# Performance work log

Hardware: AMD Instinct MI355X
Metric: run time of the kernel (lower is better)

Reference implementation:

```python
import jax, jax.numpy as jnp
import numpy as np

HEADS = 8
DIM_HEAD = 64
WINDOW = 512
SCALE = DIM_HEAD ** -0.5


def setup_inputs() -> dict:
    key = jax.random.key(0)
    k1, k2, k3 = jax.random.split(key, 3)
    b, dim, n = 2, 256, 32768
    hidden = HEADS * DIM_HEAD  # 512
    x = jax.random.normal(k1, (b, dim, n), dtype=jnp.float32)
    # Conv1d(dim, hidden*3, 1, bias=False) weight -> [3*hidden, dim]
    w_qkv = jax.random.normal(k2, (3 * hidden, dim), dtype=jnp.float32) * (dim ** -0.5)
    # Conv1d(hidden, dim, 1) weight/bias
    w_out = jax.random.normal(k3, (dim, hidden), dtype=jnp.float32) * (hidden ** -0.5)
    b_out = jnp.zeros((dim,), dtype=jnp.float32)
    return {"x": x, "w_qkv": w_qkv, "w_out": w_out, "b_out": b_out}


def reference(x, w_qkv, w_out, b_out):
    b, c, n = x.shape
    h, d, w = HEADS, DIM_HEAD, WINDOW
    nw = n // w  # n chosen divisible by window size
    # 1x1 conv == channel matmul
    qkv = jnp.einsum('oc,bcn->bon', w_qkv, x)  # [b, 3*h*d, n]
    q, k, v = jnp.split(qkv, 3, axis=1)
    # [b, h, d, nw, w]
    def to_windows(t):
        return t.reshape(b, h, d, nw, w)
    q = to_windows(q) * SCALE
    k = to_windows(k)
    v = to_windows(v)
    # non-overlapping local windows: block-diagonal attention
    sim = jnp.einsum('bhdni,bhdnj->bhnij', q, k)        # [b,h,nw,w,w]
    attn = jax.nn.softmax(sim, axis=-1)
    out = jnp.einsum('bhnij,bhdnj->bhdni', attn, v)      # [b,h,d,nw,w]
    out = out.reshape(b, h * d, n)
    return jnp.einsum('oc,bcn->bon', w_out, out) + b_out[None, :, None]
```

## Files before the change

kernel.cpp:

```cpp
#include <hip/hip_runtime.h>
#include <stdint.h>
#include <stddef.h>


typedef _Float16 f16;
typedef _Float16 half8 __attribute__((ext_vector_type(8)));
typedef float f32x4 __attribute__((ext_vector_type(4)));

#define NSEQ 32768
#define NTOT 65536
#define WIN  512

__device__ __forceinline__ void async_copy16(const f16* g, f16* l) {
  __builtin_amdgcn_global_load_lds(
      (const __attribute__((address_space(1))) void*)g,
      (__attribute__((address_space(3))) void*)l, 16, 0, 0);
}

__device__ __forceinline__ int packrtz(float a, float b) {
  typedef __fp16 fp16v2 __attribute__((ext_vector_type(2)));
  fp16v2 h = __builtin_amdgcn_cvt_pkrtz(a, b);
  return __builtin_bit_cast(int, h);
}

__global__ __launch_bounds__(256) void convert_w(
    const float* __restrict__ wqkv, const float* __restrict__ wout,
    f16* __restrict__ wqh, f16* __restrict__ woh) {
  int idx = blockIdx.x * 256 + threadIdx.x;
  if (idx < 1536 * 256) {
    float v = wqkv[idx];
    if (idx < 512 * 256) v *= 0.18033688011112042f;
    wqh[idx] = (f16)v;
  } else {
    int j = idx - 1536 * 256;
    if (j < 256 * 512) woh[j] = (f16)wout[j];
  }
}

__global__ __launch_bounds__(256) void transpose_x(
    const float* __restrict__ x, f16* __restrict__ xT) {
  __shared__ alignas(16) float tile[32][33];
  const int tx = threadIdx.x & 31, ty = threadIdx.x >> 5;
  const int bx = blockIdx.x, by = blockIdx.y;
  const float* xb = x + (size_t)blockIdx.z * 256 * NSEQ;
  f16* xTb = xT + (size_t)blockIdx.z * NSEQ * 256;
#pragma unroll
  for (int r = 0; r < 4; ++r) {
    int c = by * 32 + ty + r * 8;
    int n = bx * 32 + tx;
    tile[ty + r * 8][tx] = xb[(size_t)c * NSEQ + n];
  }
  __syncthreads();
  const int tx16 = threadIdx.x & 15, ty16 = threadIdx.x >> 4;
#pragma unroll
  for (int r = 0; r < 2; ++r) {
    int n = bx * 32 + ty16 + r * 16;
    int c = by * 32 + tx16 * 2;
    union {
      f16 h[2];
      int i;
    } u;
    u.h[0] = (f16)tile[tx16 * 2][ty16 + r * 16];
    u.h[1] = (f16)tile[tx16 * 2 + 1][ty16 + r * 16];
    *(int*)(xTb + (size_t)n * 256 + c) = u.i;
  }
}

template <int MODE, int SWZ>
__global__ __launch_bounds__(256) void gemm_k(
    const f16* __restrict__ A, const f16* __restrict__ Bm,
    void* __restrict__ outp, const float* __restrict__ bias, int K,
    int bstride, int ostride) {
  __shared__ alignas(16) f16 As[2][8192];
  __shared__ alignas(16) f16 Bs[2][8192];
  const int tid = threadIdx.x;
  const int lane = tid & 63, wid = tid >> 6;
  const int quad = lane >> 4, lid = lane & 15;

  int colb, rowb;
  if (SWZ) {
    int lin = blockIdx.y * 8 + blockIdx.x;
    int x = lin & 7, s = lin >> 3;
    colb = s & 7;
    rowb = x * 64 + (s >> 3);
  } else {
    colb = blockIdx.x;
    rowb = blockIdx.y;
  }
  const int row0 = rowb * 128, col0 = colb * 128;
  const int wm = (wid >> 1) * 64, wn = (wid & 1) * 64;

  f32x4 acc[4][4];
  const f32x4 zero = {0.f, 0.f, 0.f, 0.f};
#pragma unroll
  for (int i = 0; i < 4; ++i)
#pragma unroll
    for (int j = 0; j < 4; ++j) acc[i][j] = zero;

  const int kIters = K >> 6;

  auto stage = [&](int kt, int buf) {
    const int k0 = kt * 64;
#pragma unroll
    for (int rd = 0; rd < 4; ++rd) {
      int slot = rd * 256 + tid;
      int r = slot & 127, kc = slot >> 7;
      async_copy16(A + (size_t)(row0 + r) * K + k0 + kc * 8,
                   &As[buf][slot * 8]);
      async_copy16(Bm + (size_t)(col0 + r) * bstride + k0 + kc * 8,
                   &Bs[buf][slot * 8]);
    }
  };

  stage(0, 0);
  int p = 0;
  for (int kt = 0; kt < kIters; ++kt) {
    __syncthreads();
    if (kt + 1 < kIters) stage(kt + 1, p ^ 1);

    half8 af[2][4], bf[2][4];
#pragma unroll
    for (int ks = 0; ks < 2; ++ks) {
#pragma unroll
      for (int mi = 0; mi < 4; ++mi)
        af[ks][mi] = *(const half8*)(&As[p][((ks * 4 + quad) * 128 + wm +
                                             mi * 16 + lid) * 8]);
#pragma unroll
      for (int ni = 0; ni < 4; ++ni)
        bf[ks][ni] = *(const half8*)(&Bs[p][((ks * 4 + quad) * 128 + wn +
                                             ni * 16 + lid) * 8]);
    }
#pragma unroll
    for (int ks = 0; ks < 2; ++ks)
#pragma unroll
      for (int mi = 0; mi < 4; ++mi)
#pragma unroll
        for (int ni = 0; ni < 4; ++ni)
          acc[mi][ni] = __builtin_amdgcn_mfma_f32_16x16x32_f16(
              af[ks][mi], bf[ks][ni], acc[mi][ni], 0, 0, 0);
    p ^= 1;
  }

#pragma unroll
  for (int mi = 0; mi < 4; ++mi) {
#pragma unroll
    for (int r = 0; r < 4; ++r) {
      int grow = row0 + wm + mi * 16 + quad * 4 + r;
#pragma unroll
      for (int ni = 0; ni < 4; ++ni) {
        int gcol = col0 + wn + ni * 16 + lid;
        float v = acc[mi][ni][r];
        if (MODE == 2) {
          ((float*)outp)[(size_t)(gcol >> 15) * (256u * 32768u) +
                         (size_t)grow * 32768 + (gcol & 32767)] =
              v + bias[grow];
        } else {
          ((f16*)outp)[(size_t)grow * ostride + gcol] = (f16)v;
        }
      }
    }
  }
}

__global__ __launch_bounds__(512, 2) void attn_k(
    const f16* __restrict__ qk, const f16* __restrict__ vws,
    f16* __restrict__ ows) {
  __shared__ alignas(16) f16 smem[16384];

  const int tid = threadIdx.x;
  const int lane = tid & 63, wid = tid >> 6;
  const int quad = lane >> 4, lid = lane & 15;
  const int win = blockIdx.x;
  const int h = blockIdx.y;
  const size_t nbase = (size_t)blockIdx.z * NSEQ + (size_t)win * WIN;
  const int iw0 = wid * 64;

  half8 aq[4][2];
#pragma unroll
  for (int ig = 0; ig < 4; ++ig)
#pragma unroll
    for (int ks = 0; ks < 2; ++ks)
      aq[ig][ks] = *(const half8*)(qk + (nbase + iw0 + ig * 16 + lid) * 1024 +
                                   h * 64 + ks * 32 + quad * 8);

  f32x4 OT[4][4];
  const f32x4 zero = {0.f, 0.f, 0.f, 0.f};
#pragma unroll
  for (int di = 0; di < 4; ++di)
#pragma unroll
    for (int ig = 0; ig < 4; ++ig) OT[di][ig] = zero;
  float l_run[4] = {0.f, 0.f, 0.f, 0.f};

  const int sa = tid & 63, sc = tid >> 6;
  const int psa = (sa & 32) | ((sa & 12) << 1) | ((sa >> 2) & 4) | (sa & 3);

  async_copy16(qk + (nbase + psa) * 1024 + 512 + h * 64 + sc * 8,
               smem + tid * 8);
  async_copy16(vws + (size_t)(h * 64 + sa) * NTOT + nbase + sc * 8,
               smem + 4096 + tid * 8);

  int p = 0;
  for (int jt = 0; jt < 8; ++jt) {
    __syncthreads();
    if (jt < 7) {
      const int j0n = (jt + 1) * 64;
      f16* Kb = smem + (1 - p) * 8192;
      async_copy16(qk + (nbase + j0n + psa) * 1024 + 512 + h * 64 + sc * 8,
                   Kb + tid * 8);
      async_copy16(vws + (size_t)(h * 64 + sa) * NTOT + nbase + j0n + sc * 8,
                   Kb + 4096 + tid * 8);
    }
    const f16* Ks = smem + p * 8192;
    const f16* Vs = smem + p * 8192 + 4096;

    f32x4 sT[4][4];
#pragma unroll
    for (int jg = 0; jg < 4; ++jg)
#pragma unroll
      for (int ig = 0; ig < 4; ++ig) sT[jg][ig] = zero;
#pragma unroll
    for (int ks = 0; ks < 2; ++ks)
#pragma unroll
      for (int jg = 0; jg < 4; ++jg) {
        half8 bk =
            *(const half8*)(Ks + ((ks * 4 + quad) * 64 + jg * 16 + lid) * 8);
#pragma unroll
        for (int ig = 0; ig < 4; ++ig)
          sT[jg][ig] = __builtin_amdgcn_mfma_f32_16x16x32_f16(
              bk, aq[ig][ks], sT[jg][ig], 0, 0, 0);
      }

    int pk[4][4][2];
#pragma unroll
    for (int jg = 0; jg < 4; ++jg)
#pragma unroll
      for (int ig = 0; ig < 4; ++ig) {
        float e0 = __builtin_amdgcn_exp2f(sT[jg][ig][0]);
        float e1 = __builtin_amdgcn_exp2f(sT[jg][ig][1]);
        float e2 = __builtin_amdgcn_exp2f(sT[jg][ig][2]);
        float e3 = __builtin_amdgcn_exp2f(sT[jg][ig][3]);
        l_run[ig] += (e0 + e1) + (e2 + e3);
        pk[jg][ig][0] = packrtz(e0, e1);
        pk[jg][ig][1] = packrtz(e2, e3);
      }

#pragma unroll
    for (int ks2 = 0; ks2 < 2; ++ks2) {
      const int ta = ks2 * 2, tb = ta + 1;
      half8 pt[4];
#pragma unroll
      for (int ig = 0; ig < 4; ++ig) {
        union {
          int i[4];
          half8 h;
        } u;
        u.i[0] = pk[ta][ig][0];
        u.i[1] = pk[ta][ig][1];
        u.i[2] = pk[tb][ig][0];
        u.i[3] = pk[tb][ig][1];
        pt[ig] = u.h;
      }
#pragma unroll
      for (int di = 0; di < 4; ++di) {
        half8 av =
            *(const half8*)(Vs + ((ks2 * 4 + quad) * 64 + di * 16 + lid) * 8);
#pragma unroll
        for (int ig = 0; ig < 4; ++ig)
          OT[di][ig] = __builtin_amdgcn_mfma_f32_16x16x32_f16(
              av, pt[ig], OT[di][ig], 0, 0, 0);
      }
    }
    p ^= 1;
  }

#pragma unroll
  for (int ig = 0; ig < 4; ++ig) {
    l_run[ig] += __shfl_xor(l_run[ig], 16, 64);
    l_run[ig] += __shfl_xor(l_run[ig], 32, 64);
  }

#pragma unroll
  for (int ig = 0; ig < 4; ++ig) {
    float inv = 1.0f / l_run[ig];
    size_t rowb = (nbase + iw0 + ig * 16 + lid) * 1024 + h * 64;
#pragma unroll
    for (int di = 0; di < 4; ++di) {
      int2 o;
      o.x = packrtz(OT[di][ig][0] * inv, OT[di][ig][1] * inv);
      o.y = packrtz(OT[di][ig][2] * inv, OT[di][ig][3] * inv);
      *(int2*)(ows + rowb + di * 16 + quad * 4) = o;
    }
  }
}

extern "C" void kernel_launch(void* const* d_in, const int* in_sizes, int n_in,
                              void* d_out, int out_size, void* d_ws,
                              size_t ws_size, hipStream_t stream) {
  const float* x = (const float*)d_in[0];
  const float* w_qkv = (const float*)d_in[1];
  const float* w_out = (const float*)d_in[2];
  const float* b_out = (const float*)d_in[3];

  char* ws = (char*)d_ws;
  f16* qkw = (f16*)(ws);
  f16* vw = (f16*)(ws + 134217728);
  f16* xT = (f16*)(ws + 201326592);
  f16* wqh = (f16*)(ws + 234881024);
  f16* woh = (f16*)(ws + 235667456);

  convert_w<<<2048, 256, 0, stream>>>(w_qkv, w_out, wqh, woh);
  transpose_x<<<dim3(1024, 8, 2), 256, 0, stream>>>(x, xT);
  gemm_k<0, 1><<<dim3(8, 512), 256, 0, stream>>>(xT, wqh, qkw, nullptr, 256,
                                                 256, 1024);
  gemm_k<0, 0><<<dim3(512, 4), 256, 0, stream>>>(wqh + 1024 * 256, xT, vw,
                                                 nullptr, 256, 256, NTOT);
  attn_k<<<dim3(64, 8, 2), 512, 0, stream>>>(qkw, vw, qkw);
  gemm_k<2, 0><<<dim3(512, 2), 256, 0, stream>>>(woh, qkw, d_out, b_out, 512,
                                                 1024, 0);
}
```

Measured before the change: 393.1 us.

## Split attention window across two 256-thread blocks instead of one 512-thread block

The attention kernel now launches twice as many blocks of 256 threads, and each block handles half of the query rows in a window. Each block stages the full K/V tiles itself, with two async copies per thread. This aims for finer-grained scheduling and more resident blocks per CU. The cost is that K/V for each window is loaded twice from global memory and LDS is duplicated per block.

```diff
diff --git a/kernel.cpp b/kernel.cpp
--- a/kernel.cpp
+++ b/kernel.cpp
@@ -162,7 +162,7 @@
   }
 }
 
-__global__ __launch_bounds__(512, 2) void attn_k(
+__global__ __launch_bounds__(256, 4) void attn_k(
     const f16* __restrict__ qk, const f16* __restrict__ vws,
     f16* __restrict__ ows) {
   __shared__ alignas(16) f16 smem[16384];
@@ -170,10 +170,12 @@
   const int tid = threadIdx.x;
   const int lane = tid & 63, wid = tid >> 6;
   const int quad = lane >> 4, lid = lane & 15;
-  const int win = blockIdx.x;
+  const int bx = blockIdx.x;
+  const int win = bx & 63;
+  const int half = bx >> 6;
   const int h = blockIdx.y;
   const size_t nbase = (size_t)blockIdx.z * NSEQ + (size_t)win * WIN;
-  const int iw0 = wid * 64;
+  const int iw0 = half * 256 + wid * 64;
 
   half8 aq[4][2];
 #pragma unroll
@@ -191,25 +193,26 @@
     for (int ig = 0; ig < 4; ++ig) OT[di][ig] = zero;
   float l_run[4] = {0.f, 0.f, 0.f, 0.f};
 
-  const int sa = tid & 63, sc = tid >> 6;
-  const int psa = (sa & 32) | ((sa & 12) << 1) | ((sa >> 2) & 4) | (sa & 3);
-
-  async_copy16(qk + (nbase + psa) * 1024 + 512 + h * 64 + sc * 8,
-               smem + tid * 8);
-  async_copy16(vws + (size_t)(h * 64 + sa) * NTOT + nbase + sc * 8,
-               smem + 4096 + tid * 8);
+  auto stage = [&](int j0, f16* Kb) {
+#pragma unroll
+    for (int c = 0; c < 2; ++c) {
+      int slot = c * 256 + tid;
+      int sa = slot & 63, sc = slot >> 6;
+      int psa = (sa & 32) | ((sa & 12) << 1) | ((sa >> 2) & 4) | (sa & 3);
+      async_copy16(qk + (nbase + j0 + psa) * 1024 + 512 + h * 64 + sc * 8,
+                   Kb + slot * 8);
+      async_copy16(vws + (size_t)(h * 64 + sa) * NTOT + nbase + j0 + sc * 8,
+                   Kb + 4096 + slot * 8);
+    }
+  };
+
+  stage(0, smem);
 
   int p = 0;
   for (int jt = 0; jt < 8; ++jt) {
     __syncthreads();
-    if (jt < 7) {
-      const int j0n = (jt + 1) * 64;
-      f16* Kb = smem + (1 - p) * 8192;
-      async_copy16(qk + (nbase + j0n + psa) * 1024 + 512 + h * 64 + sc * 8,
-                   Kb + tid * 8);
-      async_copy16(vws + (size_t)(h * 64 + sa) * NTOT + nbase + j0n + sc * 8,
-                   Kb + 4096 + tid * 8);
-    }
+    if (jt < 7)
+      stage((jt + 1) * 64, smem + (1 - p) * 8192);
     const f16* Ks = smem + p * 8192;
     const f16* Vs = smem + p * 8192 + 4096;
 
@@ -314,7 +317,7 @@
                                                  256, 1024);
   gemm_k<0, 0><<<dim3(512, 4), 256, 0, stream>>>(wqh + 1024 * 256, xT, vw,
                                                  nullptr, 256, 256, NTOT);
-  attn_k<<<dim3(64, 8, 2), 512, 0, stream>>>(qkw, vw, qkw);
+  attn_k<<<dim3(128, 8, 2), 256, 0, stream>>>(qkw, vw, qkw);
   gemm_k<2, 0><<<dim3(512, 2), 256, 0, stream>>>(woh, qkw, d_out, b_out, 512,
                                                  1024, 0);
 }
```

Result: slower. 766.2 us (+94.9%).

## Quad-buffer K/V tiles, two tiles per barrier, with MFMA priority hints

Applied to the files above, without the earlier changes.

Grows the attention kernel's LDS staging from two to four 64-key K/V buffers. Each barrier now prefetches the next two tiles and computes two, which halves the number of __syncthreads per window. It also wraps the MFMA sections in s_setprio to favour matrix issue over the exp/pack phase. LDS use per block doubles to 64 KB, which at 2 blocks per CU may limit occupancy.

```diff
diff --git a/kernel.cpp b/kernel.cpp
--- a/kernel.cpp
+++ b/kernel.cpp
@@ -165,7 +165,7 @@
 __global__ __launch_bounds__(512, 2) void attn_k(
     const f16* __restrict__ qk, const f16* __restrict__ vws,
     f16* __restrict__ ows) {
-  __shared__ alignas(16) f16 smem[16384];
+  __shared__ alignas(16) f16 smem[32768];
 
   const int tid = threadIdx.x;
   const int lane = tid & 63, wid = tid >> 6;
@@ -194,83 +194,92 @@
   const int sa = tid & 63, sc = tid >> 6;
   const int psa = (sa & 32) | ((sa & 12) << 1) | ((sa >> 2) & 4) | (sa & 3);
 
-  async_copy16(qk + (nbase + psa) * 1024 + 512 + h * 64 + sc * 8,
-               smem + tid * 8);
-  async_copy16(vws + (size_t)(h * 64 + sa) * NTOT + nbase + sc * 8,
-               smem + 4096 + tid * 8);
-
-  int p = 0;
-  for (int jt = 0; jt < 8; ++jt) {
+  auto stage = [&](int jt) {
+    f16* Kb = smem + (jt & 3) * 8192;
+    const int j0 = jt * 64;
+    async_copy16(qk + (nbase + j0 + psa) * 1024 + 512 + h * 64 + sc * 8,
+                 Kb + tid * 8);
+    async_copy16(vws + (size_t)(h * 64 + sa) * NTOT + nbase + j0 + sc * 8,
+                 Kb + 4096 + tid * 8);
+  };
+
+  stage(0);
+  stage(1);
+
+  for (int s = 0; s < 4; ++s) {
     __syncthreads();
-    if (jt < 7) {
-      const int j0n = (jt + 1) * 64;
-      f16* Kb = smem + (1 - p) * 8192;
-      async_copy16(qk + (nbase + j0n + psa) * 1024 + 512 + h * 64 + sc * 8,
-                   Kb + tid * 8);
-      async_copy16(vws + (size_t)(h * 64 + sa) * NTOT + nbase + j0n + sc * 8,
-                   Kb + 4096 + tid * 8);
-    }
-    const f16* Ks = smem + p * 8192;
-    const f16* Vs = smem + p * 8192 + 4096;
-
-    f32x4 sT[4][4];
-#pragma unroll
-    for (int jg = 0; jg < 4; ++jg)
-#pragma unroll
-      for (int ig = 0; ig < 4; ++ig) sT[jg][ig] = zero;
-#pragma unroll
-    for (int ks = 0; ks < 2; ++ks)
-#pragma unroll
-      for (int jg = 0; jg < 4; ++jg) {
-        half8 bk =
-            *(const half8*)(Ks + ((ks * 4 + quad) * 64 + jg * 16 + lid) * 8);
-#pragma unroll
-        for (int ig = 0; ig < 4; ++ig)
-          sT[jg][ig] = __builtin_amdgcn_mfma_f32_16x16x32_f16(
-              bk, aq[ig][ks], sT[jg][ig], 0, 0, 0);
+    if (s < 3) {
+      stage(2 * s + 2);
+      stage(2 * s + 3);
+    }
+#pragma unroll
+    for (int t = 0; t < 2; ++t) {
+      const int jt = 2 * s + t;
+      const f16* Ks = smem + (jt & 3) * 8192;
+      const f16* Vs = Ks + 4096;
+
+      f32x4 sT[4][4];
+#pragma unroll
+      for (int jg = 0; jg < 4; ++jg)
+#pragma unroll
+        for (int ig = 0; ig < 4; ++ig) sT[jg][ig] = zero;
+      __builtin_amdgcn_s_setprio(1);
+#pragma unroll
+      for (int ks = 0; ks < 2; ++ks)
+#pragma unroll
+        for (int jg = 0; jg < 4; ++jg) {
+          half8 bk =
+              *(const half8*)(Ks + ((ks * 4 + quad) * 64 + jg * 16 + lid) * 8);
+#pragma unroll
+          for (int ig = 0; ig < 4; ++ig)
+            sT[jg][ig] = __builtin_amdgcn_mfma_f32_16x16x32_f16(
+                bk, aq[ig][ks], sT[jg][ig], 0, 0, 0);
+        }
+      __builtin_amdgcn_s_setprio(0);
+
+      int pk[4][4][2];
+#pragma unroll
+      for (int jg = 0; jg < 4; ++jg)
+#pragma unroll
+        for (int ig = 0; ig < 4; ++ig) {
+          float e0 = __builtin_amdgcn_exp2f(sT[jg][ig][0]);
+          float e1 = __builtin_amdgcn_exp2f(sT[jg][ig][1]);
+          float e2 = __builtin_amdgcn_exp2f(sT[jg][ig][2]);
+          float e3 = __builtin_amdgcn_exp2f(sT[jg][ig][3]);
+          l_run[ig] += (e0 + e1) + (e2 + e3);
+          pk[jg][ig][0] = packrtz(e0, e1);
+          pk[jg][ig][1] = packrtz(e2, e3);
+        }
+
+      __builtin_amdgcn_s_setprio(1);
+#pragma unroll
+      for (int ks2 = 0; ks2 < 2; ++ks2) {
+        const int ta = ks2 * 2, tb = ta + 1;
+        half8 pt[4];
+#pragma unroll
+        for (int ig = 0; ig < 4; ++ig) {
+          union {
+            int i[4];
+            half8 h;
+          } u;
+          u.i[0] = pk[ta][ig][0];
+          u.i[1] = pk[ta][ig][1];
+          u.i[2] = pk[tb][ig][0];
+          u.i[3] = pk[tb][ig][1];
+          pt[ig] = u.h;
+        }
+#pragma unroll
+        for (int di = 0; di < 4; ++di) {
+          half8 av =
+              *(const half8*)(Vs + ((ks2 * 4 + quad) * 64 + di * 16 + lid) * 8);
+#pragma unroll
+          for (int ig = 0; ig < 4; ++ig)
+            OT[di][ig] = __builtin_amdgcn_mfma_f32_16x16x32_f16(
+                av, pt[ig], OT[di][ig], 0, 0, 0);
+        }
       }
-
-    int pk[4][4][2];
-#pragma unroll
-    for (int jg = 0; jg < 4; ++jg)
-#pragma unroll
-      for (int ig = 0; ig < 4; ++ig) {
-        float e0 = __builtin_amdgcn_exp2f(sT[jg][ig][0]);
-        float e1 = __builtin_amdgcn_exp2f(sT[jg][ig][1]);
-        float e2 = __builtin_amdgcn_exp2f(sT[jg][ig][2]);
-        float e3 = __builtin_amdgcn_exp2f(sT[jg][ig][3]);
-        l_run[ig] += (e0 + e1) + (e2 + e3);
-        pk[jg][ig][0] = packrtz(e0, e1);
-        pk[jg][ig][1] = packrtz(e2, e3);
-      }
-
-#pragma unroll
-    for (int ks2 = 0; ks2 < 2; ++ks2) {
-      const int ta = ks2 * 2, tb = ta + 1;
-      half8 pt[4];
-#pragma unroll
-      for (int ig = 0; ig < 4; ++ig) {
-        union {
-          int i[4];
-          half8 h;
-        } u;
-        u.i[0] = pk[ta][ig][0];
-        u.i[1] = pk[ta][ig][1];
-        u.i[2] = pk[tb][ig][0];
-        u.i[3] = pk[tb][ig][1];
-        pt[ig] = u.h;
-      }
-#pragma unroll
-      for (int di = 0; di < 4; ++di) {
-        half8 av =
-            *(const half8*)(Vs + ((ks2 * 4 + quad) * 64 + di * 16 + lid) * 8);
-#pragma unroll
-        for (int ig = 0; ig < 4; ++ig)
-          OT[di][ig] = __builtin_amdgcn_mfma_f32_16x16x32_f16(
-              av, pt[ig], OT[di][ig], 0, 0, 0);
-      }
-    }
-    p ^= 1;
+      __builtin_amdgcn_s_setprio(0);
+    }
   }
 
 #pragma unroll
```

Result: slower. 508.5 us (+29.4%).
